# Optimization experiments

Hardware: AMD Instinct MI355X
Metric: run time of the kernel (lower is better)

Reference implementation:

```python
import jax, jax.numpy as jnp
import numpy as np

N = 50000      # nodes
E = 400000     # edges (avg degree 8)
N_IN = 256     # n_in_chan
N_HID = 256    # n_hid_chan


def gcn_conv(x, src, dst, W, b, n):
    """PyG GCNConv: D^{-1/2}(A+I)D^{-1/2} X W^T + b (add_self_loops=True, unit weights)."""
    h = x @ W.T                                           # [n, out]
    # degree over A + I: each node has a self loop (the initial ones) plus in-edges
    deg = jnp.ones((n,), h.dtype).at[dst].add(1.0)        # [n]
    dinv = jax.lax.rsqrt(deg)                             # deg >= 1 always
    norm = dinv[src] * dinv[dst]                          # [E]
    agg = jnp.zeros_like(h).at[dst].add(h[src] * norm[:, None])
    agg = agg + h * (dinv * dinv)[:, None]                # self-loop term, norm = dinv_i^2
    return agg + b


def setup_inputs() -> dict:
    key = jax.random.key(0)
    k1, k2, k3, k4 = jax.random.split(key, 4)
    x = jax.random.normal(k1, (N, N_IN + N_HID), dtype=jnp.float32)
    edge_index = jax.random.randint(k2, (2, E), 0, N, dtype=jnp.int64)
    s1 = 1.0 / np.sqrt(N_IN + N_HID)
    s2 = 1.0 / np.sqrt(N_HID)
    W1 = jax.random.normal(k3, (N_HID, N_IN + N_HID), dtype=jnp.float32) * s1
    W2 = jax.random.normal(k4, (N_HID, N_HID), dtype=jnp.float32) * s2
    b1 = jnp.zeros((N_HID,), jnp.float32)
    b2 = jnp.zeros((N_HID,), jnp.float32)
    return {"x": x, "edge_index": edge_index, "W1": W1, "b1": b1, "W2": W2, "b2": b2}


def reference(x, edge_index, W1, b1, W2, b2):
    src, dst = edge_index[0], edge_index[1]
    h = jax.nn.relu(gcn_conv(x, src, dst, W1, b1, N))
    return gcn_conv(h, src, dst, W2, b2, N)
```

## Files before the change

### kernel.cpp

```cpp
#include <hip/hip_runtime.h>

#define NN 50000
#define CH 256

typedef unsigned short u16;
typedef unsigned int   u32;

using short8 = __attribute__((ext_vector_type(8))) short;
using u16x8  = __attribute__((ext_vector_type(8))) unsigned short;
using f32x4  = __attribute__((ext_vector_type(4))) float;

static __device__ __forceinline__ float4 ld4(const float* p){ return *(const float4*)p; }

static __device__ __forceinline__ u16 f2b(float f){
  u32 u = __float_as_uint(f);
  u = (u + 0x7fffu + ((u >> 16) & 1u)) >> 16;
  return (u16)u;
}
static __device__ __forceinline__ float b2f(u16 b){
  return __uint_as_float(((u32)b) << 16);
}


__global__ void hist_kernel(const int* __restrict__ dst, int* __restrict__ cnt, int E){
  int e = blockIdx.x*256 + threadIdx.x;
  if (e < E) atomicAdd(&cnt[dst[e]], 1);
}

__global__ void scan_partial_kernel(const int* __restrict__ cnt, int* __restrict__ bsum,
                                    float* __restrict__ dinv, int n){
  __shared__ int sd[256];
  int t = threadIdx.x;
  int base = blockIdx.x*1024 + t*4;
  int s = 0;
  #pragma unroll
  for (int j=0;j<4;j++){
    int idx = base+j;
    if (idx<n){
      int v = cnt[idx];
      s += v;
      dinv[idx] = rsqrtf(1.0f + (float)v);
    }
  }
  sd[t] = s; __syncthreads();
  for (int off=128; off>0; off>>=1){ if (t<off) sd[t]+=sd[t+off]; __syncthreads(); }
  if (t==0) bsum[blockIdx.x] = sd[0];
}

__global__ void scan_bsums_kernel(int* __restrict__ bsum, int nb){
  int t = threadIdx.x;
  int v = (t < nb) ? bsum[t] : 0;
  int orig = v;
  #pragma unroll
  for (int off=1; off<64; off<<=1){
    int u = __shfl_up(v, off, 64);
    if (t >= off) v += u;
  }
  if (t < nb) bsum[t] = v - orig;
}

__global__ void scan_final_kernel(const int* __restrict__ cnt, const int* __restrict__ bsum,
                                  int* __restrict__ offs, int* __restrict__ cursor, int n, int total){
  __shared__ int sd[256];
  int t = threadIdx.x;
  int base = blockIdx.x*1024 + t*4;
  int v[4]; int s=0;
  #pragma unroll
  for (int j=0;j<4;j++){ int idx=base+j; v[j] = (idx<n)?cnt[idx]:0; s += v[j]; }
  sd[t]=s; __syncthreads();
  for (int off=1; off<256; off<<=1){
    int x = (t>=off)? sd[t-off] : 0;
    __syncthreads();
    sd[t] += x;
    __syncthreads();
  }
  int run = bsum[blockIdx.x] + sd[t] - s;
  #pragma unroll
  for (int j=0;j<4;j++){
    int idx=base+j;
    if (idx<n){ offs[idx]=run; cursor[idx]=run; }
    run += v[j];
  }
  if (blockIdx.x==0 && t==0) offs[n] = total;
}

__global__ void scatter_kernel(const int* __restrict__ src, const int* __restrict__ dst,
                               const float* __restrict__ dinv, int* __restrict__ cursor,
                               int* __restrict__ esrc, float* __restrict__ enorm, int E){
  int e = blockIdx.x*256 + threadIdx.x;
  if (e < E){
    int d = dst[e], s = src[e];
    int pos = atomicAdd(&cursor[d], 1);
    esrc[pos] = s;
    enorm[pos] = dinv[s]*dinv[d];
  }
}


__global__ __launch_bounds__(256) void cvt_all_kernel(const float* __restrict__ x,  u16* __restrict__ Xbf,  int xn4,
                                                      const float* __restrict__ w1, u16* __restrict__ W1bf, int w1n4,
                                                      const float* __restrict__ w2, u16* __restrict__ W2bf, int w2n4){
  int T = gridDim.x * 256;
  int g = blockIdx.x*256 + threadIdx.x;
  for (int i = g; i < xn4; i += T){
    float4 v = ld4(x + (size_t)i*4);
    ushort4 o; o.x=f2b(v.x); o.y=f2b(v.y); o.z=f2b(v.z); o.w=f2b(v.w);
    *(ushort4*)(Xbf + (size_t)i*4) = o;
  }
  for (int i = g; i < w1n4; i += T){
    float4 v = ld4(w1 + (size_t)i*4);
    ushort4 o; o.x=f2b(v.x); o.y=f2b(v.y); o.z=f2b(v.z); o.w=f2b(v.w);
    *(ushort4*)(W1bf + (size_t)i*4) = o;
  }
  for (int i = g; i < w2n4; i += T){
    float4 v = ld4(w2 + (size_t)i*4);
    ushort4 o; o.x=f2b(v.x); o.y=f2b(v.y); o.z=f2b(v.z); o.w=f2b(v.w);
    *(ushort4*)(W2bf + (size_t)i*4) = o;
  }
}


static __device__ __forceinline__ void gload_lds16(const u16* g, u16* l){
  __builtin_amdgcn_global_load_lds((const __attribute__((address_space(1))) void*)g,
                                   (__attribute__((address_space(3))) void*)l, 16, 0, 0);
}

__global__ __launch_bounds__(256) void gemm_mfma_kernel(const u16* __restrict__ A,
                                                        const u16* __restrict__ B,
                                                        u16* __restrict__ C,
                                                        int M, int K){
  __shared__ u16 As[128*32];
  __shared__ u16 Bs[128*32];
  int tid = threadIdx.x;
  int wave = tid >> 6, lane = tid & 63;
  int bm = blockIdx.x, bn = blockIdx.y;

  int sr = tid >> 2;
  int sc = (tid & 3) * 8;
  int ar0 = bm*128 + sr;       if (ar0 > M-1) ar0 = M-1;
  int ar1 = bm*128 + 64 + sr;  if (ar1 > M-1) ar1 = M-1;
  const u16* ga0 = A + (size_t)ar0*K + sc;
  const u16* ga1 = A + (size_t)ar1*K + sc;
  const u16* gb0 = B + (size_t)(bn*128 + sr)*K + sc;
  const u16* gb1 = B + (size_t)(bn*128 + 64 + sr)*K + sc;
  u16* la0 = As + (size_t)(wave*64)*8;
  u16* la1 = As + (size_t)(256 + wave*64)*8;
  u16* lb0 = Bs + (size_t)(wave*64)*8;
  u16* lb1 = Bs + (size_t)(256 + wave*64)*8;

  int wm = wave & 1, wn = wave >> 1;
  int lm = lane & 15;
  int lk = (lane >> 4) * 8;

  f32x4 acc[4][4] = {};

  for (int k0 = 0; k0 < K; k0 += 32){
    gload_lds16(ga0 + k0, la0);
    gload_lds16(ga1 + k0, la1);
    gload_lds16(gb0 + k0, lb0);
    gload_lds16(gb1 + k0, lb1);
    __syncthreads();
    short8 af[4], bfr[4];
    #pragma unroll
    for (int i=0;i<4;i++)
      af[i] = *(const short8*)&As[(size_t)(wm*64 + i*16 + lm)*32 + lk];
    #pragma unroll
    for (int j=0;j<4;j++)
      bfr[j] = *(const short8*)&Bs[(size_t)(wn*64 + j*16 + lm)*32 + lk];
    #pragma unroll
    for (int i=0;i<4;i++)
      #pragma unroll
      for (int j=0;j<4;j++)
        acc[i][j] = __builtin_amdgcn_mfma_f32_16x16x32_bf16(af[i], bfr[j], acc[i][j], 0, 0, 0);
    __syncthreads();
  }

  int rb = (lane >> 4) * 4;
  #pragma unroll
  for (int i=0;i<4;i++){
    #pragma unroll
    for (int r=0;r<4;r++){
      int row = bm*128 + wm*64 + i*16 + rb + r;
      if (row < M){
        #pragma unroll
        for (int j=0;j<4;j++){
          int col = bn*128 + wn*64 + j*16 + lm;
          C[(size_t)row*CH + col] = f2b(acc[i][j][r]);
        }
      }
    }
  }
}


template<bool RELU, bool OUTBF>
__global__ __launch_bounds__(256) void aggregate_kernel(const u16* __restrict__ h,
                                                        const float* __restrict__ bias,
                                                        const float* __restrict__ dinv,
                                                        const int* __restrict__ offs,
                                                        const int* __restrict__ esrc,
                                                        const float* __restrict__ enorm,
                                                        void* __restrict__ outv, int n){
  int wave = threadIdx.x >> 6;
  int lane = threadIdx.x & 63;
  int i = blockIdx.x*4 + wave;
  if (i >= n) return;
  int half = lane >> 5;
  int c = (lane & 31) * 8;

  float acc[8];
  #pragma unroll
  for (int k=0;k<8;k++) acc[k] = 0.f;

  int e0 = offs[i], e1 = offs[i+1];
  int e = e0 + half;
  for (; e + 6 < e1; e += 8){
    int s0 = esrc[e],   s1 = esrc[e+2], s2 = esrc[e+4], s3 = esrc[e+6];
    float n0 = enorm[e], n1 = enorm[e+2], n2 = enorm[e+4], n3 = enorm[e+6];
    u16x8 h0 = *(const u16x8*)(h + (size_t)s0*CH + c);
    u16x8 h1 = *(const u16x8*)(h + (size_t)s1*CH + c);
    u16x8 h2 = *(const u16x8*)(h + (size_t)s2*CH + c);
    u16x8 h3 = *(const u16x8*)(h + (size_t)s3*CH + c);
    #pragma unroll
    for (int k=0;k<8;k++) acc[k] += b2f(h0[k])*n0;
    #pragma unroll
    for (int k=0;k<8;k++) acc[k] += b2f(h1[k])*n1;
    #pragma unroll
    for (int k=0;k<8;k++) acc[k] += b2f(h2[k])*n2;
    #pragma unroll
    for (int k=0;k<8;k++) acc[k] += b2f(h3[k])*n3;
  }
  for (; e < e1; e += 2){
    int s0 = esrc[e];
    float n0 = enorm[e];
    u16x8 h0 = *(const u16x8*)(h + (size_t)s0*CH + c);
    #pragma unroll
    for (int k=0;k<8;k++) acc[k] += b2f(h0[k])*n0;
  }

  if (half == 0){
    float di = dinv[i];
    float w = di*di;
    float4 b0 = ld4(bias + c), b1 = ld4(bias + c + 4);
    u16x8 hv = *(const u16x8*)(h + (size_t)i*CH + c);
    acc[0] += b2f(hv[0])*w + b0.x; acc[1] += b2f(hv[1])*w + b0.y;
    acc[2] += b2f(hv[2])*w + b0.z; acc[3] += b2f(hv[3])*w + b0.w;
    acc[4] += b2f(hv[4])*w + b1.x; acc[5] += b2f(hv[5])*w + b1.y;
    acc[6] += b2f(hv[6])*w + b1.z; acc[7] += b2f(hv[7])*w + b1.w;
  }

  #pragma unroll
  for (int k=0;k<8;k++) acc[k] += __shfl_xor(acc[k], 32, 64);

  if (half == 0){
    if (RELU){
      #pragma unroll
      for (int k=0;k<8;k++) acc[k] = fmaxf(acc[k], 0.f);
    }
    if (OUTBF){
      u16x8 o;
      #pragma unroll
      for (int k=0;k<8;k++) o[k] = f2b(acc[k]);
      *(u16x8*)((u16*)outv + (size_t)i*CH + c) = o;
    } else {
      float* op = (float*)outv + (size_t)i*CH + c;
      *(float4*)op       = make_float4(acc[0],acc[1],acc[2],acc[3]);
      *(float4*)(op + 4) = make_float4(acc[4],acc[5],acc[6],acc[7]);
    }
  }
}


extern "C" void kernel_launch(void* const* d_in, const int* in_sizes, int n_in,
                              void* d_out, int out_size, void* d_ws, size_t ws_size,
                              hipStream_t stream){
  const float* x  = (const float*)d_in[0];
  const int*   ei = (const int*)d_in[1];
  const float* W1 = (const float*)d_in[2];
  const float* b1 = (const float*)d_in[3];
  const float* W2 = (const float*)d_in[4];
  const float* b2 = (const float*)d_in[5];
  float* out = (float*)d_out;

  const int n = NN;
  const int E = in_sizes[1] / 2;
  const int* src = ei;
  const int* dst = ei + E;
  const int KIN = in_sizes[0] / n;

  char* ws = (char*)d_ws;
  size_t off = 0;
  auto alloc = [&](size_t bytes)->char* {
    char* p = ws + off;
    off += (bytes + 255) & ~(size_t)255;
    return p;
  };
  u16*   Xbf    = (u16*)  alloc((size_t)n*KIN*sizeof(u16));
  u16*   W1bf   = (u16*)  alloc((size_t)CH*KIN*sizeof(u16));
  u16*   W2bf   = (u16*)  alloc((size_t)CH*CH*sizeof(u16));
  float* dinv   = (float*)alloc((size_t)n*sizeof(float));
  int*   cnt    = (int*)  alloc((size_t)n*sizeof(int));
  int*   offs   = (int*)  alloc((size_t)(n+1)*sizeof(int));
  int*   cursor = (int*)  alloc((size_t)n*sizeof(int));
  int*   bsum   = (int*)  alloc(256*sizeof(int));
  int*   esrc   = (int*)  alloc((size_t)E*sizeof(int));
  float* enorm  = (float*)alloc((size_t)E*sizeof(float));
  (void)ws_size;

  u16* g1out = (u16*)d_out;
  u16* h1bf  = Xbf;
  u16* g2out = Xbf + (size_t)n*CH;

  hipMemsetAsync(cnt, 0, (size_t)n*sizeof(int), stream);
  hist_kernel<<<(E+255)/256, 256, 0, stream>>>(dst, cnt, E);
  int nb = (n + 1023) / 1024;
  scan_partial_kernel<<<nb, 256, 0, stream>>>(cnt, bsum, dinv, n);
  scan_bsums_kernel<<<1, 64, 0, stream>>>(bsum, nb);
  scan_final_kernel<<<nb, 256, 0, stream>>>(cnt, bsum, offs, cursor, n, E);
  scatter_kernel<<<(E+255)/256, 256, 0, stream>>>(src, dst, dinv, cursor, esrc, enorm, E);

  cvt_all_kernel<<<512, 256, 0, stream>>>(x, Xbf, n*KIN/4, W1, W1bf, CH*KIN/4, W2, W2bf, CH*CH/4);

  dim3 gg((n+127)/128, CH/128);
  gemm_mfma_kernel<<<gg, 256, 0, stream>>>(Xbf, W1bf, g1out, n, KIN);
  aggregate_kernel<true, true><<<(n+3)/4, 256, 0, stream>>>(g1out, b1, dinv, offs, esrc, enorm, h1bf, n);

  gemm_mfma_kernel<<<gg, 256, 0, stream>>>(h1bf, W2bf, g2out, n, CH);
  aggregate_kernel<false, false><<<(n+3)/4, 256, 0, stream>>>(g2out, b2, dinv, offs, esrc, enorm, out, n);
}
```

Before: 355.2 us.

## Fuse fp32-to-bf16 conversion into first GEMM and collapse scan kernels

The first GEMM now reads fp32 X and W1 directly and converts to bf16 while staging tiles into LDS, so the separate pass that wrote a bf16 copy of X is gone. The three-kernel scan becomes one kernel in which each block re-sums all preceding counts. The W2 conversion moves into the histogram kernel. Edge norms are now computed in the aggregation kernels from dinv instead of being stored per edge. In exchange, the GEMM reads twice the bytes for A and drops the async global-to-LDS load path, and the scan does redundant prefix work.

```diff
diff --git a/kernel.cpp b/kernel.cpp
--- a/kernel.cpp
+++ b/kernel.cpp
@@ -22,100 +22,153 @@
 }
 
 
-__global__ void hist_kernel(const int* __restrict__ dst, int* __restrict__ cnt, int E){
-  int e = blockIdx.x*256 + threadIdx.x;
-  if (e < E) atomicAdd(&cnt[dst[e]], 1);
-}
-
-__global__ void scan_partial_kernel(const int* __restrict__ cnt, int* __restrict__ bsum,
-                                    float* __restrict__ dinv, int n){
+__global__ void hist_kernel(const int* __restrict__ dst, int* __restrict__ cnt, int E,
+                            const float* __restrict__ W2, u16* __restrict__ W2bf, int w2n4){
+  int T = gridDim.x * 256;
+  int g = blockIdx.x*256 + threadIdx.x;
+  if (g < E) atomicAdd(&cnt[dst[g]], 1);
+  for (int i = g; i < w2n4; i += T){
+    float4 v = ld4(W2 + (size_t)i*4);
+    ushort4 o; o.x=f2b(v.x); o.y=f2b(v.y); o.z=f2b(v.z); o.w=f2b(v.w);
+    *(ushort4*)(W2bf + (size_t)i*4) = o;
+  }
+}
+
+
+__global__ __launch_bounds__(256) void scanfused_kernel(const int* __restrict__ cnt,
+                                                        float* __restrict__ dinv,
+                                                        int* __restrict__ offs,
+                                                        int* __restrict__ cursor,
+                                                        int n, int E){
   __shared__ int sd[256];
-  int t = threadIdx.x;
-  int base = blockIdx.x*1024 + t*4;
+  __shared__ int sbase;
+  int t = threadIdx.x, b = blockIdx.x;
+
+  int lim = b*1024;
   int s = 0;
-  #pragma unroll
-  for (int j=0;j<4;j++){
-    int idx = base+j;
-    if (idx<n){
-      int v = cnt[idx];
-      s += v;
-      dinv[idx] = rsqrtf(1.0f + (float)v);
-    }
+  for (int i = t*4; i < lim; i += 1024){
+    int4 v = *(const int4*)(cnt + i);
+    s += v.x + v.y + v.z + v.w;
   }
   sd[t] = s; __syncthreads();
   for (int off=128; off>0; off>>=1){ if (t<off) sd[t]+=sd[t+off]; __syncthreads(); }
-  if (t==0) bsum[blockIdx.x] = sd[0];
-}
-
-__global__ void scan_bsums_kernel(int* __restrict__ bsum, int nb){
-  int t = threadIdx.x;
-  int v = (t < nb) ? bsum[t] : 0;
-  int orig = v;
-  #pragma unroll
-  for (int off=1; off<64; off<<=1){
-    int u = __shfl_up(v, off, 64);
-    if (t >= off) v += u;
-  }
-  if (t < nb) bsum[t] = v - orig;
-}
-
-__global__ void scan_final_kernel(const int* __restrict__ cnt, const int* __restrict__ bsum,
-                                  int* __restrict__ offs, int* __restrict__ cursor, int n, int total){
-  __shared__ int sd[256];
-  int t = threadIdx.x;
-  int base = blockIdx.x*1024 + t*4;
-  int v[4]; int s=0;
-  #pragma unroll
-  for (int j=0;j<4;j++){ int idx=base+j; v[j] = (idx<n)?cnt[idx]:0; s += v[j]; }
-  sd[t]=s; __syncthreads();
+  if (t==0) sbase = sd[0];
+  __syncthreads();
+  int base = sbase;
+  __syncthreads();
+
+  int idx0 = b*1024 + t*4;
+  int v[4]; int ls = 0;
+  #pragma unroll
+  for (int j=0;j<4;j++){
+    int idx = idx0 + j;
+    v[j] = (idx < n) ? cnt[idx] : 0;
+    if (idx < n) dinv[idx] = rsqrtf(1.0f + (float)v[j]);
+    ls += v[j];
+  }
+  sd[t] = ls; __syncthreads();
+  #pragma unroll
   for (int off=1; off<256; off<<=1){
-    int x = (t>=off)? sd[t-off] : 0;
+    int x = (t>=off) ? sd[t-off] : 0;
     __syncthreads();
     sd[t] += x;
     __syncthreads();
   }
-  int run = bsum[blockIdx.x] + sd[t] - s;
+  int run = base + sd[t] - ls;
   #pragma unroll
   for (int j=0;j<4;j++){
-    int idx=base+j;
-    if (idx<n){ offs[idx]=run; cursor[idx]=run; }
+    int idx = idx0 + j;
+    if (idx < n){ offs[idx] = run; cursor[idx] = run; }
     run += v[j];
   }
-  if (blockIdx.x==0 && t==0) offs[n] = total;
-}
+  if (b==0 && t==0) offs[n] = E;
+}
+
 
 __global__ void scatter_kernel(const int* __restrict__ src, const int* __restrict__ dst,
-                               const float* __restrict__ dinv, int* __restrict__ cursor,
-                               int* __restrict__ esrc, float* __restrict__ enorm, int E){
+                               int* __restrict__ cursor, int* __restrict__ esrc, int E){
   int e = blockIdx.x*256 + threadIdx.x;
   if (e < E){
-    int d = dst[e], s = src[e];
+    int d = dst[e];
     int pos = atomicAdd(&cursor[d], 1);
-    esrc[pos] = s;
-    enorm[pos] = dinv[s]*dinv[d];
-  }
-}
-
-
-__global__ __launch_bounds__(256) void cvt_all_kernel(const float* __restrict__ x,  u16* __restrict__ Xbf,  int xn4,
-                                                      const float* __restrict__ w1, u16* __restrict__ W1bf, int w1n4,
-                                                      const float* __restrict__ w2, u16* __restrict__ W2bf, int w2n4){
-  int T = gridDim.x * 256;
-  int g = blockIdx.x*256 + threadIdx.x;
-  for (int i = g; i < xn4; i += T){
-    float4 v = ld4(x + (size_t)i*4);
-    ushort4 o; o.x=f2b(v.x); o.y=f2b(v.y); o.z=f2b(v.z); o.w=f2b(v.w);
-    *(ushort4*)(Xbf + (size_t)i*4) = o;
-  }
-  for (int i = g; i < w1n4; i += T){
-    float4 v = ld4(w1 + (size_t)i*4);
-    ushort4 o; o.x=f2b(v.x); o.y=f2b(v.y); o.z=f2b(v.z); o.w=f2b(v.w);
-    *(ushort4*)(W1bf + (size_t)i*4) = o;
-  }
-  for (int i = g; i < w2n4; i += T){
-    float4 v = ld4(w2 + (size_t)i*4);
-    ushort4 o; o.x=f2b(v.x); o.y=f2b(v.y); o.z=f2b(v.z); o.w=f2b(v.w);
-    *(ushort4*)(W2bf + (size_t)i*4) = o;
+    esrc[pos] = src[e];
+  }
+}
+
+
+__global__ __launch_bounds__(256) void gemm_mfma_f32in_kernel(const float* __restrict__ A,
+                                                              const float* __restrict__ B,
+                                                              u16* __restrict__ C,
+                                                              int M, int K){
+  __shared__ u16 As[128*32];
+  __shared__ u16 Bs[128*32];
+  int tid = threadIdx.x;
+  int wave = tid >> 6, lane = tid & 63;
+  int bm = blockIdx.x, bn = blockIdx.y;
+
+  int sr = tid >> 2;
+  int sc = (tid & 3) * 8;
+  int rA0 = bm*128 + sr;       if (rA0 > M-1) rA0 = M-1;
+  int rA1 = bm*128 + 64 + sr;  if (rA1 > M-1) rA1 = M-1;
+  const float* ga0 = A + (size_t)rA0*K + sc;
+  const float* ga1 = A + (size_t)rA1*K + sc;
+  const float* gb0 = B + (size_t)(bn*128 + sr)*K + sc;
+  const float* gb1 = B + (size_t)(bn*128 + 64 + sr)*K + sc;
+
+  int wm = wave & 1, wn = wave >> 1;
+  int lm = lane & 15;
+  int lk = (lane >> 4) * 8;
+
+  f32x4 acc[4][4] = {};
+
+  for (int k0 = 0; k0 < K; k0 += 32){
+    float4 a00 = ld4(ga0 + k0), a01 = ld4(ga0 + k0 + 4);
+    float4 a10 = ld4(ga1 + k0), a11 = ld4(ga1 + k0 + 4);
+    float4 b00 = ld4(gb0 + k0), b01 = ld4(gb0 + k0 + 4);
+    float4 b10 = ld4(gb1 + k0), b11 = ld4(gb1 + k0 + 4);
+    u16x8 wa0, wa1, wb0, wb1;
+    wa0[0]=f2b(a00.x); wa0[1]=f2b(a00.y); wa0[2]=f2b(a00.z); wa0[3]=f2b(a00.w);
+    wa0[4]=f2b(a01.x); wa0[5]=f2b(a01.y); wa0[6]=f2b(a01.z); wa0[7]=f2b(a01.w);
+    wa1[0]=f2b(a10.x); wa1[1]=f2b(a10.y); wa1[2]=f2b(a10.z); wa1[3]=f2b(a10.w);
+    wa1[4]=f2b(a11.x); wa1[5]=f2b(a11.y); wa1[6]=f2b(a11.z); wa1[7]=f2b(a11.w);
+    wb0[0]=f2b(b00.x); wb0[1]=f2b(b00.y); wb0[2]=f2b(b00.z); wb0[3]=f2b(b00.w);
+    wb0[4]=f2b(b01.x); wb0[5]=f2b(b01.y); wb0[6]=f2b(b01.z); wb0[7]=f2b(b01.w);
+    wb1[0]=f2b(b10.x); wb1[1]=f2b(b10.y); wb1[2]=f2b(b10.z); wb1[3]=f2b(b10.w);
+    wb1[4]=f2b(b11.x); wb1[5]=f2b(b11.y); wb1[6]=f2b(b11.z); wb1[7]=f2b(b11.w);
+    *(u16x8*)&As[(size_t)sr*32 + sc]        = wa0;
+    *(u16x8*)&As[(size_t)(64+sr)*32 + sc]   = wa1;
+    *(u16x8*)&Bs[(size_t)sr*32 + sc]        = wb0;
+    *(u16x8*)&Bs[(size_t)(64+sr)*32 + sc]   = wb1;
+    __syncthreads();
+    short8 af[4], bfr[4];
+    #pragma unroll
+    for (int i=0;i<4;i++)
+      af[i] = *(const short8*)&As[(size_t)(wm*64 + i*16 + lm)*32 + lk];
+    #pragma unroll
+    for (int j=0;j<4;j++)
+      bfr[j] = *(const short8*)&Bs[(size_t)(wn*64 + j*16 + lm)*32 + lk];
+    #pragma unroll
+    for (int i=0;i<4;i++)
+      #pragma unroll
+      for (int j=0;j<4;j++)
+        acc[i][j] = __builtin_amdgcn_mfma_f32_16x16x32_bf16(af[i], bfr[j], acc[i][j], 0, 0, 0);
+    __syncthreads();
+  }
+
+  int rb = (lane >> 4) * 4;
+  #pragma unroll
+  for (int i=0;i<4;i++){
+    #pragma unroll
+    for (int r=0;r<4;r++){
+      int row = bm*128 + wm*64 + i*16 + rb + r;
+      if (row < M){
+        #pragma unroll
+        for (int j=0;j<4;j++){
+          int col = bn*128 + wn*64 + j*16 + lm;
+          C[(size_t)row*CH + col] = f2b(acc[i][j][r]);
+        }
+      }
+    }
   }
 }
 
@@ -199,7 +252,6 @@
                                                         const float* __restrict__ dinv,
                                                         const int* __restrict__ offs,
                                                         const int* __restrict__ esrc,
-                                                        const float* __restrict__ enorm,
                                                         void* __restrict__ outv, int n){
   int wave = threadIdx.x >> 6;
   int lane = threadIdx.x & 63;
@@ -207,6 +259,7 @@
   if (i >= n) return;
   int half = lane >> 5;
   int c = (lane & 31) * 8;
+  float di = dinv[i];
 
   float acc[8];
   #pragma unroll
@@ -216,7 +269,7 @@
   int e = e0 + half;
   for (; e + 6 < e1; e += 8){
     int s0 = esrc[e],   s1 = esrc[e+2], s2 = esrc[e+4], s3 = esrc[e+6];
-    float n0 = enorm[e], n1 = enorm[e+2], n2 = enorm[e+4], n3 = enorm[e+6];
+    float n0 = dinv[s0]*di, n1 = dinv[s1]*di, n2 = dinv[s2]*di, n3 = dinv[s3]*di;
     u16x8 h0 = *(const u16x8*)(h + (size_t)s0*CH + c);
     u16x8 h1 = *(const u16x8*)(h + (size_t)s1*CH + c);
     u16x8 h2 = *(const u16x8*)(h + (size_t)s2*CH + c);
@@ -232,14 +285,13 @@
   }
   for (; e < e1; e += 2){
     int s0 = esrc[e];
-    float n0 = enorm[e];
+    float n0 = dinv[s0]*di;
     u16x8 h0 = *(const u16x8*)(h + (size_t)s0*CH + c);
     #pragma unroll
     for (int k=0;k<8;k++) acc[k] += b2f(h0[k])*n0;
   }
 
   if (half == 0){
-    float di = dinv[i];
     float w = di*di;
     float4 b0 = ld4(bias + c), b1 = ld4(bias + c + 4);
     u16x8 hv = *(const u16x8*)(h + (size_t)i*CH + c);
@@ -295,36 +347,28 @@
     off += (bytes + 255) & ~(size_t)255;
     return p;
   };
-  u16*   Xbf    = (u16*)  alloc((size_t)n*KIN*sizeof(u16));
-  u16*   W1bf   = (u16*)  alloc((size_t)CH*KIN*sizeof(u16));
+  u16*   h1bf   = (u16*)  alloc((size_t)n*CH*sizeof(u16));
+  u16*   g2out  = (u16*)  alloc((size_t)n*CH*sizeof(u16));
   u16*   W2bf   = (u16*)  alloc((size_t)CH*CH*sizeof(u16));
   float* dinv   = (float*)alloc((size_t)n*sizeof(float));
   int*   cnt    = (int*)  alloc((size_t)n*sizeof(int));
   int*   offs   = (int*)  alloc((size_t)(n+1)*sizeof(int));
   int*   cursor = (int*)  alloc((size_t)n*sizeof(int));
-  int*   bsum   = (int*)  alloc(256*sizeof(int));
   int*   esrc   = (int*)  alloc((size_t)E*sizeof(int));
-  float* enorm  = (float*)alloc((size_t)E*sizeof(float));
   (void)ws_size;
 
   u16* g1out = (u16*)d_out;
-  u16* h1bf  = Xbf;
-  u16* g2out = Xbf + (size_t)n*CH;
 
   hipMemsetAsync(cnt, 0, (size_t)n*sizeof(int), stream);
-  hist_kernel<<<(E+255)/256, 256, 0, stream>>>(dst, cnt, E);
+  hist_kernel<<<(E+255)/256, 256, 0, stream>>>(dst, cnt, E, W2, W2bf, CH*CH/4);
   int nb = (n + 1023) / 1024;
-  scan_partial_kernel<<<nb, 256, 0, stream>>>(cnt, bsum, dinv, n);
-  scan_bsums_kernel<<<1, 64, 0, stream>>>(bsum, nb);
-  scan_final_kernel<<<nb, 256, 0, stream>>>(cnt, bsum, offs, cursor, n, E);
-  scatter_kernel<<<(E+255)/256, 256, 0, stream>>>(src, dst, dinv, cursor, esrc, enorm, E);
-
-  cvt_all_kernel<<<512, 256, 0, stream>>>(x, Xbf, n*KIN/4, W1, W1bf, CH*KIN/4, W2, W2bf, CH*CH/4);
+  scanfused_kernel<<<nb, 256, 0, stream>>>(cnt, dinv, offs, cursor, n, E);
+  scatter_kernel<<<(E+255)/256, 256, 0, stream>>>(src, dst, cursor, esrc, E);
 
   dim3 gg((n+127)/128, CH/128);
-  gemm_mfma_kernel<<<gg, 256, 0, stream>>>(Xbf, W1bf, g1out, n, KIN);
-  aggregate_kernel<true, true><<<(n+3)/4, 256, 0, stream>>>(g1out, b1, dinv, offs, esrc, enorm, h1bf, n);
+  gemm_mfma_f32in_kernel<<<gg, 256, 0, stream>>>(x, W1, g1out, n, KIN);
+  aggregate_kernel<true, true><<<(n+3)/4, 256, 0, stream>>>(g1out, b1, dinv, offs, esrc, h1bf, n);
 
   gemm_mfma_kernel<<<gg, 256, 0, stream>>>(h1bf, W2bf, g2out, n, CH);
-  aggregate_kernel<false, false><<<(n+3)/4, 256, 0, stream>>>(g2out, b2, dinv, offs, esrc, enorm, out, n);
-}
+  aggregate_kernel<false, false><<<(n+3)/4, 256, 0, stream>>>(g2out, b2, dinv, offs, esrc, out, n);
+}
```

Result: faster. 341.7 us (-3.8%).
